# Optimization experiments

Measured on AMD Instinct MI355X. Metric: run time of the kernel, lower is better.

## Reference

```python
import math
import jax, jax.numpy as jnp
import numpy as np

D_MODEL = 2048
NUM_HEADS = 16

def setup_inputs() -> dict:
    key = jax.random.key(0)
    k1, k2, k3, k4, k5 = jax.random.split(key, 5)
    s = 1.0 / math.sqrt(D_MODEL)
    return {
        "in_features": jax.random.normal(k1, (2, 2048, D_MODEL), dtype=jnp.float32),
        "q_proj": jax.random.normal(k2, (D_MODEL, D_MODEL), dtype=jnp.float32) * s,
        "k_proj": jax.random.normal(k3, (D_MODEL, D_MODEL), dtype=jnp.float32) * s,
        "v_proj": jax.random.normal(k4, (D_MODEL, D_MODEL), dtype=jnp.float32) * s,
        "o_proj": jax.random.normal(k5, (D_MODEL, D_MODEL), dtype=jnp.float32) * s,
    }

def reference(in_features, q_proj, k_proj, v_proj, o_proj):
    B, S, D = in_features.shape
    H = NUM_HEADS
    d_k = D // H
    # x @ W.T, then split heads: [B, H, S, d_k]
    def proj(W):
        return (in_features @ W.T).reshape(B, S, H, d_k).transpose(0, 2, 1, 3)
    Q, K, V = proj(q_proj), proj(k_proj), proj(v_proj)
    scores = jnp.einsum("bhqd,bhkd->bhqk", Q, K) / math.sqrt(d_k)
    causal = jnp.triu(jnp.ones((S, S), dtype=bool), k=1)  # True above diagonal
    scores = jnp.where(causal, -jnp.inf, scores)
    attn = jax.nn.softmax(scores, axis=-1)
    out = jnp.einsum("bhqk,bhkd->bhqd", attn, V)
    out = out.transpose(0, 2, 1, 3).reshape(B, S, D)
    return out @ o_proj.T
```

## Files before the change

### kernel.cpp

```cpp
#include <hip/hip_runtime.h>
#include <math.h>
#include <stdint.h>

#define D_MODEL 2048
#define NHEAD   16
#define DK      128
#define SEQ     2048
#define BATCH   2
#define MROWS   (BATCH * SEQ)

typedef __bf16 bf16;
typedef __bf16 bf16x8 __attribute__((ext_vector_type(8)));
typedef __bf16 bf16x4 __attribute__((ext_vector_type(4)));
typedef float  f32x4  __attribute__((ext_vector_type(4)));

__device__ __forceinline__ bf16 f2bf(float f) {
    unsigned u = __builtin_bit_cast(unsigned, f);
    u += 0x7fffu + ((u >> 16) & 1u);
    unsigned short h = (unsigned short)(u >> 16);
    return __builtin_bit_cast(bf16, h);
}

#define GLDS16(gp, lp)                                                        \
    __builtin_amdgcn_global_load_lds(                                         \
        (__attribute__((address_space(1))) void*)(uintptr_t)(gp),             \
        (__attribute__((address_space(3))) void*)(lp), 16, 0, 0)

__global__ void cvt_f32_bf16(const float* __restrict__ src,
                             bf16* __restrict__ dst, int n4) {
    int i = blockIdx.x * blockDim.x + threadIdx.x;
    if (i < n4) {
        float4 v = ((const float4*)src)[i];
        bf16x4 o;
        o[0] = f2bf(v.x); o[1] = f2bf(v.y); o[2] = f2bf(v.z); o[3] = f2bf(v.w);
        *(bf16x4*)(dst + (size_t)i * 4) = o;
    }
}

template <int EPI>
__global__ __launch_bounds__(256)
void gemm_bt(const bf16* __restrict__ A, const bf16* __restrict__ B,
             void* __restrict__ Cv, int M, int N, int K) {
    __shared__ alignas(16) bf16 sA[128 * 32];
    __shared__ alignas(16) bf16 sB[128 * 32];

    const int tid  = threadIdx.x;
    const int lane = tid & 63;
    const int wid  = tid >> 6;
    const int wm   = wid >> 1, wn = wid & 1;
    const int brow = blockIdx.y * 128, bcol = blockIdx.x * 128;
    const int r16  = lane & 15, g = lane >> 4;

    f32x4 acc[4][4] = {};

    const int c0 = tid, c1 = 256 + tid;
    const int rowS0 = c0 >> 2, colS0 = (c0 & 3) * 8;
    const int rowS1 = c1 >> 2, colS1 = (c1 & 3) * 8;

    for (int kt = 0; kt < K; kt += 32) {
        GLDS16(A + (size_t)(brow + rowS0) * K + kt + colS0, &sA[c0 * 8]);
        GLDS16(A + (size_t)(brow + rowS1) * K + kt + colS1, &sA[c1 * 8]);
        GLDS16(B + (size_t)(bcol + rowS0) * K + kt + colS0, &sB[c0 * 8]);
        GLDS16(B + (size_t)(bcol + rowS1) * K + kt + colS1, &sB[c1 * 8]);
        __syncthreads();

        bf16x8 af[4], bfr[4];
#pragma unroll
        for (int m = 0; m < 4; ++m)
            af[m] = *(const bf16x8*)&sA[(wm * 64 + m * 16 + r16) * 32 + g * 8];
#pragma unroll
        for (int n = 0; n < 4; ++n)
            bfr[n] = *(const bf16x8*)&sB[(wn * 64 + n * 16 + r16) * 32 + g * 8];
#pragma unroll
        for (int m = 0; m < 4; ++m)
#pragma unroll
            for (int n = 0; n < 4; ++n)
                acc[m][n] = __builtin_amdgcn_mfma_f32_16x16x32_bf16(
                    af[m], bfr[n], acc[m][n], 0, 0, 0);
        __syncthreads();
    }

#pragma unroll
    for (int m = 0; m < 4; ++m) {
#pragma unroll
        for (int n = 0; n < 4; ++n) {
            const int col  = bcol + wn * 64 + n * 16 + r16;
            const int row0 = brow + wm * 64 + m * 16 + g * 4;
            if constexpr (EPI == 0) {
                bf16* C = (bf16*)Cv;
#pragma unroll
                for (int r = 0; r < 4; ++r)
                    C[(size_t)(row0 + r) * N + col] = f2bf(acc[m][n][r]);
            } else if constexpr (EPI == 1) {
                float* C = (float*)Cv;
#pragma unroll
                for (int r = 0; r < 4; ++r)
                    C[(size_t)(row0 + r) * N + col] = acc[m][n][r];
            } else {
                bf16* C = (bf16*)Cv;
                const int b = row0 >> 11, s = row0 & 2047;
                bf16x4 v;
#pragma unroll
                for (int r = 0; r < 4; ++r) v[r] = f2bf(acc[m][n][r]);
                *(bf16x4*)&C[(size_t)(b * 2048 + col) * 2048 + s] = v;
            }
        }
    }
}

__global__ __launch_bounds__(256)
void attn_fwd(const bf16* __restrict__ Q, const bf16* __restrict__ Kb,
              const bf16* __restrict__ Vt, bf16* __restrict__ AO) {
    __shared__ alignas(16) bf16 P_lds[4][32][40];

    const int tid  = threadIdx.x;
    const int lane = tid & 63;
    const int wid  = tid >> 6;
    const int r16  = lane & 15, g = lane >> 4;
    const int bh   = blockIdx.y;
    const int b    = bh >> 4;
    const int NT   = SEQ / 128;
    const int qt   = (blockIdx.y & 16) ? (NT - 1 - (int)blockIdx.x)
                                       : (int)blockIdx.x;
    const int qbase = qt * 128 + wid * 32;
    const size_t rowbase = (size_t)b * SEQ;
    const int hcol = (bh & 15) * DK;
    const float scale = 0.08838834764831845f;

    bf16x8 aq[2][4];
#pragma unroll
    for (int m = 0; m < 2; ++m) {
        const bf16* qp =
            Q + (rowbase + qbase + m * 16 + r16) * D_MODEL + hcol + g * 8;
#pragma unroll
        for (int c = 0; c < 4; ++c) aq[m][c] = *(const bf16x8*)(qp + c * 32);
    }

    f32x4 o[2][8] = {};
    float m_run[2][4], l_run[2][4];
#pragma unroll
    for (int m = 0; m < 2; ++m)
#pragma unroll
        for (int r = 0; r < 4; ++r) {
            m_run[m][r] = -INFINITY;
            l_run[m][r] = 0.f;
        }

    const int ntile = (qbase >> 5) + 1;
    for (int t = 0; t < ntile; ++t) {
        const int kv0 = t * 32;
        f32x4 s[2][2] = {};
#pragma unroll
        for (int n = 0; n < 2; ++n) {
            const bf16* kp =
                Kb + (rowbase + kv0 + n * 16 + r16) * D_MODEL + hcol + g * 8;
#pragma unroll
            for (int c = 0; c < 4; ++c) {
                bf16x8 bk = *(const bf16x8*)(kp + c * 32);
#pragma unroll
                for (int m = 0; m < 2; ++m)
                    s[m][n] = __builtin_amdgcn_mfma_f32_16x16x32_bf16(
                        aq[m][c], bk, s[m][n], 0, 0, 0);
            }
        }
#pragma unroll
        for (int m = 0; m < 2; ++m)
#pragma unroll
            for (int n = 0; n < 2; ++n)
#pragma unroll
                for (int r = 0; r < 4; ++r) s[m][n][r] *= scale;

        if (kv0 + 31 > qbase) {
#pragma unroll
            for (int m = 0; m < 2; ++m)
#pragma unroll
                for (int n = 0; n < 2; ++n)
#pragma unroll
                    for (int r = 0; r < 4; ++r) {
                        int kvg = kv0 + n * 16 + r16;
                        int qg  = qbase + m * 16 + g * 4 + r;
                        if (kvg > qg) s[m][n][r] = -INFINITY;
                    }
        }

        float tm[2][4];
#pragma unroll
        for (int m = 0; m < 2; ++m)
#pragma unroll
            for (int r = 0; r < 4; ++r) tm[m][r] = fmaxf(s[m][0][r], s[m][1][r]);
#pragma unroll
        for (int d = 1; d < 16; d <<= 1)
#pragma unroll
            for (int m = 0; m < 2; ++m)
#pragma unroll
                for (int r = 0; r < 4; ++r)
                    tm[m][r] = fmaxf(tm[m][r], __shfl_xor(tm[m][r], d));

        float alpha[2][4];
#pragma unroll
        for (int m = 0; m < 2; ++m)
#pragma unroll
            for (int r = 0; r < 4; ++r) {
                float nm    = fmaxf(m_run[m][r], tm[m][r]);
                alpha[m][r] = __expf(m_run[m][r] - nm);
                m_run[m][r] = nm;
            }
#pragma unroll
        for (int m = 0; m < 2; ++m)
#pragma unroll
            for (int n = 0; n < 2; ++n)
#pragma unroll
                for (int r = 0; r < 4; ++r)
                    s[m][n][r] = __expf(s[m][n][r] - m_run[m][r]);

        float rs[2][4];
#pragma unroll
        for (int m = 0; m < 2; ++m)
#pragma unroll
            for (int r = 0; r < 4; ++r) rs[m][r] = s[m][0][r] + s[m][1][r];
#pragma unroll
        for (int d = 1; d < 16; d <<= 1)
#pragma unroll
            for (int m = 0; m < 2; ++m)
#pragma unroll
                for (int r = 0; r < 4; ++r) rs[m][r] += __shfl_xor(rs[m][r], d);
#pragma unroll
        for (int m = 0; m < 2; ++m)
#pragma unroll
            for (int r = 0; r < 4; ++r)
                l_run[m][r] = l_run[m][r] * alpha[m][r] + rs[m][r];
#pragma unroll
        for (int m = 0; m < 2; ++m)
#pragma unroll
            for (int dt = 0; dt < 8; ++dt)
#pragma unroll
                for (int r = 0; r < 4; ++r) o[m][dt][r] *= alpha[m][r];

#pragma unroll
        for (int m = 0; m < 2; ++m)
#pragma unroll
            for (int n = 0; n < 2; ++n)
#pragma unroll
                for (int r = 0; r < 4; ++r)
                    P_lds[wid][m * 16 + g * 4 + r][n * 16 + r16] =
                        f2bf(s[m][n][r]);

        bf16x8 pa[2];
#pragma unroll
        for (int m = 0; m < 2; ++m)
            pa[m] = *(const bf16x8*)&P_lds[wid][m * 16 + r16][g * 8];

        const bf16* vp = Vt + ((size_t)bh * DK) * SEQ + kv0 + g * 8;
#pragma unroll
        for (int dt = 0; dt < 8; ++dt) {
            bf16x8 bv = *(const bf16x8*)(vp + (size_t)(dt * 16 + r16) * SEQ);
#pragma unroll
            for (int m = 0; m < 2; ++m)
                o[m][dt] = __builtin_amdgcn_mfma_f32_16x16x32_bf16(
                    pa[m], bv, o[m][dt], 0, 0, 0);
        }
    }

#pragma unroll
    for (int m = 0; m < 2; ++m) {
        float rl[4];
#pragma unroll
        for (int r = 0; r < 4; ++r) rl[r] = 1.f / l_run[m][r];
#pragma unroll
        for (int dt = 0; dt < 8; ++dt)
#pragma unroll
            for (int r = 0; r < 4; ++r) {
                float val = o[m][dt][r] * rl[r];
                AO[(rowbase + qbase + m * 16 + g * 4 + r) * D_MODEL + hcol +
                   dt * 16 + r16] = f2bf(val);
            }
    }
}

extern "C" void kernel_launch(void* const* d_in, const int* in_sizes, int n_in,
                              void* d_out, int out_size, void* d_ws,
                              size_t ws_size, hipStream_t stream) {
    const float* X  = (const float*)d_in[0];
    const float* Wq = (const float*)d_in[1];
    const float* Wk = (const float*)d_in[2];
    const float* Wv = (const float*)d_in[3];
    const float* Wo = (const float*)d_in[4];

    bf16* base = (bf16*)d_ws;
    const size_t NX = (size_t)MROWS * D_MODEL;
    const size_t NW = (size_t)D_MODEL * D_MODEL;
    bf16* Xb  = base;
    bf16* Qb  = Xb + NX;
    bf16* Kbf = Qb + NX;
    bf16* Vt  = Kbf + NX;
    bf16* AOb = Vt + NX;
    bf16* Wqb = AOb + NX;
    bf16* Wkb = Wqb + NW;
    bf16* Wvb = Wkb + NW;
    bf16* Wob = Wvb + NW;

    cvt_f32_bf16<<<(int)(NX / 4 / 256), 256, 0, stream>>>(X, Xb, (int)(NX / 4));
    cvt_f32_bf16<<<(int)(NW / 4 / 256), 256, 0, stream>>>(Wq, Wqb, (int)(NW / 4));
    cvt_f32_bf16<<<(int)(NW / 4 / 256), 256, 0, stream>>>(Wk, Wkb, (int)(NW / 4));
    cvt_f32_bf16<<<(int)(NW / 4 / 256), 256, 0, stream>>>(Wv, Wvb, (int)(NW / 4));
    cvt_f32_bf16<<<(int)(NW / 4 / 256), 256, 0, stream>>>(Wo, Wob, (int)(NW / 4));

    dim3 ggrid(D_MODEL / 128, MROWS / 128);
    gemm_bt<0><<<ggrid, 256, 0, stream>>>(Xb, Wqb, Qb, MROWS, D_MODEL, D_MODEL);
    gemm_bt<0><<<ggrid, 256, 0, stream>>>(Xb, Wkb, Kbf, MROWS, D_MODEL, D_MODEL);
    gemm_bt<2><<<ggrid, 256, 0, stream>>>(Xb, Wvb, Vt, MROWS, D_MODEL, D_MODEL);

    attn_fwd<<<dim3(SEQ / 128, BATCH * NHEAD), 256, 0, stream>>>(Qb, Kbf, Vt,
                                                                 AOb);

    gemm_bt<1><<<ggrid, 256, 0, stream>>>(AOb, Wob, d_out, MROWS, D_MODEL,
                                          D_MODEL);
}
```

Baseline: 547.4 us.

## Fuse QKV projections into one GEMM and stage K tiles in LDS for attention

Merges the three Q/K/V projection GEMMs into a single launch over a concatenated 6144-column weight, selecting the output path per block. The Q scale is folded into the Q epilogue so attention no longer multiplies scores. The attention kernel now processes 64-key tiles, double-buffers K into swizzled LDS with async global-to-LDS loads, and uses a finite large negative instead of -inf. This cuts launch count, improves K reuse across warps and widens the MFMA work per tile, at the cost of more LDS and registers per block. The fused GEMM indexes Wqb as one contiguous 6144x2048 weight, which holds only because Wq, Wk and Wv are laid out back to back in the buffer.

```diff
diff --git a/kernel.cpp b/kernel.cpp
--- a/kernel.cpp
+++ b/kernel.cpp
@@ -25,6 +25,8 @@
     __builtin_amdgcn_global_load_lds(                                         \
         (__attribute__((address_space(1))) void*)(uintptr_t)(gp),             \
         (__attribute__((address_space(3))) void*)(lp), 16, 0, 0)
+
+#define QSCALE 0.08838834764831845f
 
 __global__ void cvt_f32_bf16(const float* __restrict__ src,
                              bf16* __restrict__ dst, int n4) {
@@ -37,12 +39,13 @@
     }
 }
 
-template <int EPI>
 __global__ __launch_bounds__(256)
-void gemm_bt(const bf16* __restrict__ A, const bf16* __restrict__ B,
-             void* __restrict__ Cv, int M, int N, int K) {
+void gemm_qkv(const bf16* __restrict__ A, const bf16* __restrict__ B,
+              bf16* __restrict__ Qb, bf16* __restrict__ Kbf,
+              bf16* __restrict__ Vt) {
     __shared__ alignas(16) bf16 sA[128 * 32];
     __shared__ alignas(16) bf16 sB[128 * 32];
+    const int K = D_MODEL;
 
     const int tid  = threadIdx.x;
     const int lane = tid & 63;
@@ -80,38 +83,94 @@
         __syncthreads();
     }
 
+    const int which = bcol >> 11;
 #pragma unroll
     for (int m = 0; m < 4; ++m) {
 #pragma unroll
         for (int n = 0; n < 4; ++n) {
             const int col  = bcol + wn * 64 + n * 16 + r16;
             const int row0 = brow + wm * 64 + m * 16 + g * 4;
-            if constexpr (EPI == 0) {
-                bf16* C = (bf16*)Cv;
+            if (which == 0) {
 #pragma unroll
                 for (int r = 0; r < 4; ++r)
-                    C[(size_t)(row0 + r) * N + col] = f2bf(acc[m][n][r]);
-            } else if constexpr (EPI == 1) {
-                float* C = (float*)Cv;
+                    Qb[(size_t)(row0 + r) * D_MODEL + col] =
+                        f2bf(acc[m][n][r] * QSCALE);
+            } else if (which == 1) {
 #pragma unroll
                 for (int r = 0; r < 4; ++r)
-                    C[(size_t)(row0 + r) * N + col] = acc[m][n][r];
+                    Kbf[(size_t)(row0 + r) * D_MODEL + (col - 2048)] =
+                        f2bf(acc[m][n][r]);
             } else {
-                bf16* C = (bf16*)Cv;
                 const int b = row0 >> 11, s = row0 & 2047;
                 bf16x4 v;
 #pragma unroll
                 for (int r = 0; r < 4; ++r) v[r] = f2bf(acc[m][n][r]);
-                *(bf16x4*)&C[(size_t)(b * 2048 + col) * 2048 + s] = v;
+                *(bf16x4*)&Vt[(size_t)(b * 2048 + (col - 4096)) * 2048 + s] = v;
             }
         }
     }
 }
 
 __global__ __launch_bounds__(256)
+void gemm_o(const bf16* __restrict__ A, const bf16* __restrict__ B,
+            float* __restrict__ C) {
+    __shared__ alignas(16) bf16 sA[128 * 32];
+    __shared__ alignas(16) bf16 sB[128 * 32];
+    const int K = D_MODEL, N = D_MODEL;
+
+    const int tid  = threadIdx.x;
+    const int lane = tid & 63;
+    const int wid  = tid >> 6;
+    const int wm   = wid >> 1, wn = wid & 1;
+    const int brow = blockIdx.y * 128, bcol = blockIdx.x * 128;
+    const int r16  = lane & 15, g = lane >> 4;
+
+    f32x4 acc[4][4] = {};
+
+    const int c0 = tid, c1 = 256 + tid;
+    const int rowS0 = c0 >> 2, colS0 = (c0 & 3) * 8;
+    const int rowS1 = c1 >> 2, colS1 = (c1 & 3) * 8;
+
+    for (int kt = 0; kt < K; kt += 32) {
+        GLDS16(A + (size_t)(brow + rowS0) * K + kt + colS0, &sA[c0 * 8]);
+        GLDS16(A + (size_t)(brow + rowS1) * K + kt + colS1, &sA[c1 * 8]);
+        GLDS16(B + (size_t)(bcol + rowS0) * K + kt + colS0, &sB[c0 * 8]);
+        GLDS16(B + (size_t)(bcol + rowS1) * K + kt + colS1, &sB[c1 * 8]);
+        __syncthreads();
+
+        bf16x8 af[4], bfr[4];
+#pragma unroll
+        for (int m = 0; m < 4; ++m)
+            af[m] = *(const bf16x8*)&sA[(wm * 64 + m * 16 + r16) * 32 + g * 8];
+#pragma unroll
+        for (int n = 0; n < 4; ++n)
+            bfr[n] = *(const bf16x8*)&sB[(wn * 64 + n * 16 + r16) * 32 + g * 8];
+#pragma unroll
+        for (int m = 0; m < 4; ++m)
+#pragma unroll
+            for (int n = 0; n < 4; ++n)
+                acc[m][n] = __builtin_amdgcn_mfma_f32_16x16x32_bf16(
+                    af[m], bfr[n], acc[m][n], 0, 0, 0);
+        __syncthreads();
+    }
+
+#pragma unroll
+    for (int m = 0; m < 4; ++m)
+#pragma unroll
+        for (int n = 0; n < 4; ++n) {
+            const int col  = bcol + wn * 64 + n * 16 + r16;
+            const int row0 = brow + wm * 64 + m * 16 + g * 4;
+#pragma unroll
+            for (int r = 0; r < 4; ++r)
+                C[(size_t)(row0 + r) * N + col] = acc[m][n][r];
+        }
+}
+
+__global__ __launch_bounds__(256, 2)
 void attn_fwd(const bf16* __restrict__ Q, const bf16* __restrict__ Kb,
               const bf16* __restrict__ Vt, bf16* __restrict__ AO) {
-    __shared__ alignas(16) bf16 P_lds[4][32][40];
+    __shared__ alignas(16) bf16 sK[2][64 * 128];
+    __shared__ alignas(16) bf16 P_lds[4][32][72];
 
     const int tid  = threadIdx.x;
     const int lane = tid & 63;
@@ -119,13 +178,12 @@
     const int r16  = lane & 15, g = lane >> 4;
     const int bh   = blockIdx.y;
     const int b    = bh >> 4;
-    const int NT   = SEQ / 128;
-    const int qt   = (blockIdx.y & 16) ? (NT - 1 - (int)blockIdx.x)
+    const int qt   = (blockIdx.y & 16) ? (15 - (int)blockIdx.x)
                                        : (int)blockIdx.x;
     const int qbase = qt * 128 + wid * 32;
     const size_t rowbase = (size_t)b * SEQ;
     const int hcol = (bh & 15) * DK;
-    const float scale = 0.08838834764831845f;
+    const int nt   = 2 * qt + 2;
 
     bf16x8 aq[2][4];
 #pragma unroll
@@ -142,123 +200,159 @@
     for (int m = 0; m < 2; ++m)
 #pragma unroll
         for (int r = 0; r < 4; ++r) {
-            m_run[m][r] = -INFINITY;
+            m_run[m][r] = -3.0e38f;
             l_run[m][r] = 0.f;
         }
 
-    const int ntile = (qbase >> 5) + 1;
-    for (int t = 0; t < ntile; ++t) {
-        const int kv0 = t * 32;
-        f32x4 s[2][2] = {};
-#pragma unroll
-        for (int n = 0; n < 2; ++n) {
-            const bf16* kp =
-                Kb + (rowbase + kv0 + n * 16 + r16) * D_MODEL + hcol + g * 8;
+    auto stage = [&](int buf, int t) {
+        const int kv0 = t * 64;
+#pragma unroll
+        for (int j = 0; j < 4; ++j) {
+            const int ldsOff = wid * 1024 + j * 4096 + lane * 16;
+            const int row    = ldsOff >> 8;
+            const int colB   = (lane & 15) * 16;
+            const int scolB  = colB ^ ((row & 7) << 4);
+            const bf16* gp =
+                Kb + (rowbase + kv0 + row) * D_MODEL + hcol + (scolB >> 1);
+            GLDS16(gp, (bf16*)sK[buf] + (ldsOff >> 1));
+        }
+    };
+
+    int cur = 0;
+    stage(0, 0);
+    __syncthreads();
+
+    for (int t = 0; t < nt; ++t) {
+        if (t + 1 < nt) stage(cur ^ 1, t + 1);
+        const int kv0 = t * 64;
+
+        if (kv0 <= qbase + 31) {
+            f32x4 s[2][4] = {};
 #pragma unroll
             for (int c = 0; c < 4; ++c) {
-                bf16x8 bk = *(const bf16x8*)(kp + c * 32);
+                bf16x8 kf[4];
+#pragma unroll
+                for (int n = 0; n < 4; ++n) {
+                    const int row  = n * 16 + r16;
+                    const int colB = (c * 64 + g * 16) ^ ((row & 7) << 4);
+                    kf[n] = *(const bf16x8*)&sK[cur][row * 128 + (colB >> 1)];
+                }
+#pragma unroll
+                for (int n = 0; n < 4; ++n)
+#pragma unroll
+                    for (int m = 0; m < 2; ++m)
+                        s[m][n] = __builtin_amdgcn_mfma_f32_16x16x32_bf16(
+                            aq[m][c], kf[n], s[m][n], 0, 0, 0);
+            }
+
+            if (kv0 + 63 > qbase) {
 #pragma unroll
                 for (int m = 0; m < 2; ++m)
-                    s[m][n] = __builtin_amdgcn_mfma_f32_16x16x32_bf16(
-                        aq[m][c], bk, s[m][n], 0, 0, 0);
+#pragma unroll
+                    for (int n = 0; n < 4; ++n)
+#pragma unroll
+                        for (int r = 0; r < 4; ++r) {
+                            int kvg = kv0 + n * 16 + r16;
+                            int qg  = qbase + m * 16 + g * 4 + r;
+                            if (kvg > qg) s[m][n][r] = -3.0e38f;
+                        }
+            }
+
+            float tm[2][4];
+#pragma unroll
+            for (int m = 0; m < 2; ++m)
+#pragma unroll
+                for (int r = 0; r < 4; ++r)
+                    tm[m][r] = fmaxf(fmaxf(s[m][0][r], s[m][1][r]),
+                                     fmaxf(s[m][2][r], s[m][3][r]));
+#pragma unroll
+            for (int d = 1; d < 16; d <<= 1)
+#pragma unroll
+                for (int m = 0; m < 2; ++m)
+#pragma unroll
+                    for (int r = 0; r < 4; ++r)
+                        tm[m][r] = fmaxf(tm[m][r], __shfl_xor(tm[m][r], d));
+
+            float alpha[2][4];
+#pragma unroll
+            for (int m = 0; m < 2; ++m)
+#pragma unroll
+                for (int r = 0; r < 4; ++r) {
+                    float nm    = fmaxf(m_run[m][r], tm[m][r]);
+                    alpha[m][r] = __expf(m_run[m][r] - nm);
+                    m_run[m][r] = nm;
+                }
+#pragma unroll
+            for (int m = 0; m < 2; ++m)
+#pragma unroll
+                for (int n = 0; n < 4; ++n)
+#pragma unroll
+                    for (int r = 0; r < 4; ++r)
+                        s[m][n][r] = __expf(s[m][n][r] - m_run[m][r]);
+
+            float rs[2][4];
+#pragma unroll
+            for (int m = 0; m < 2; ++m)
+#pragma unroll
+                for (int r = 0; r < 4; ++r)
+                    rs[m][r] = (s[m][0][r] + s[m][1][r]) +
+                               (s[m][2][r] + s[m][3][r]);
+#pragma unroll
+            for (int d = 1; d < 16; d <<= 1)
+#pragma unroll
+                for (int m = 0; m < 2; ++m)
+#pragma unroll
+                    for (int r = 0; r < 4; ++r)
+                        rs[m][r] += __shfl_xor(rs[m][r], d);
+#pragma unroll
+            for (int m = 0; m < 2; ++m)
+#pragma unroll
+                for (int r = 0; r < 4; ++r)
+                    l_run[m][r] = l_run[m][r] * alpha[m][r] + rs[m][r];
+#pragma unroll
+            for (int m = 0; m < 2; ++m)
+#pragma unroll
+                for (int dt = 0; dt < 8; ++dt)
+#pragma unroll
+                    for (int r = 0; r < 4; ++r) o[m][dt][r] *= alpha[m][r];
+
+#pragma unroll
+            for (int m = 0; m < 2; ++m)
+#pragma unroll
+                for (int n = 0; n < 4; ++n)
+#pragma unroll
+                    for (int r = 0; r < 4; ++r)
+                        P_lds[wid][m * 16 + g * 4 + r][n * 16 + r16] =
+                            f2bf(s[m][n][r]);
+
+            bf16x8 pa[2][2];
+#pragma unroll
+            for (int m = 0; m < 2; ++m)
+#pragma unroll
+                for (int c = 0; c < 2; ++c)
+                    pa[m][c] = *(const bf16x8*)&P_lds[wid][m * 16 + r16]
+                                                    [c * 32 + g * 8];
+
+            const bf16* vp = Vt + ((size_t)bh * DK) * SEQ + kv0 + g * 8;
+#pragma unroll
+            for (int dt = 0; dt < 8; ++dt) {
+                bf16x8 bv[2];
+#pragma unroll
+                for (int c = 0; c < 2; ++c)
+                    bv[c] = *(const bf16x8*)(vp +
+                                             (size_t)(dt * 16 + r16) * SEQ +
+                                             c * 32);
+#pragma unroll
+                for (int m = 0; m < 2; ++m)
+#pragma unroll
+                    for (int c = 0; c < 2; ++c)
+                        o[m][dt] = __builtin_amdgcn_mfma_f32_16x16x32_bf16(
+                            pa[m][c], bv[c], o[m][dt], 0, 0, 0);
             }
         }
-#pragma unroll
-        for (int m = 0; m < 2; ++m)
-#pragma unroll
-            for (int n = 0; n < 2; ++n)
-#pragma unroll
-                for (int r = 0; r < 4; ++r) s[m][n][r] *= scale;
-
-        if (kv0 + 31 > qbase) {
-#pragma unroll
-            for (int m = 0; m < 2; ++m)
-#pragma unroll
-                for (int n = 0; n < 2; ++n)
-#pragma unroll
-                    for (int r = 0; r < 4; ++r) {
-                        int kvg = kv0 + n * 16 + r16;
-                        int qg  = qbase + m * 16 + g * 4 + r;
-                        if (kvg > qg) s[m][n][r] = -INFINITY;
-                    }
-        }
-
-        float tm[2][4];
-#pragma unroll
-        for (int m = 0; m < 2; ++m)
-#pragma unroll
-            for (int r = 0; r < 4; ++r) tm[m][r] = fmaxf(s[m][0][r], s[m][1][r]);
-#pragma unroll
-        for (int d = 1; d < 16; d <<= 1)
-#pragma unroll
-            for (int m = 0; m < 2; ++m)
-#pragma unroll
-                for (int r = 0; r < 4; ++r)
-                    tm[m][r] = fmaxf(tm[m][r], __shfl_xor(tm[m][r], d));
-
-        float alpha[2][4];
-#pragma unroll
-        for (int m = 0; m < 2; ++m)
-#pragma unroll
-            for (int r = 0; r < 4; ++r) {
-                float nm    = fmaxf(m_run[m][r], tm[m][r]);
-                alpha[m][r] = __expf(m_run[m][r] - nm);
-                m_run[m][r] = nm;
-            }
-#pragma unroll
-        for (int m = 0; m < 2; ++m)
-#pragma unroll
-            for (int n = 0; n < 2; ++n)
-#pragma unroll
-                for (int r = 0; r < 4; ++r)
-                    s[m][n][r] = __expf(s[m][n][r] - m_run[m][r]);
-
-        float rs[2][4];
-#pragma unroll
-        for (int m = 0; m < 2; ++m)
-#pragma unroll
-            for (int r = 0; r < 4; ++r) rs[m][r] = s[m][0][r] + s[m][1][r];
-#pragma unroll
-        for (int d = 1; d < 16; d <<= 1)
-#pragma unroll
-            for (int m = 0; m < 2; ++m)
-#pragma unroll
-                for (int r = 0; r < 4; ++r) rs[m][r] += __shfl_xor(rs[m][r], d);
-#pragma unroll
-        for (int m = 0; m < 2; ++m)
-#pragma unroll
-            for (int r = 0; r < 4; ++r)
-                l_run[m][r] = l_run[m][r] * alpha[m][r] + rs[m][r];
-#pragma unroll
-        for (int m = 0; m < 2; ++m)
-#pragma unroll
-            for (int dt = 0; dt < 8; ++dt)
-#pragma unroll
-                for (int r = 0; r < 4; ++r) o[m][dt][r] *= alpha[m][r];
-
-#pragma unroll
-        for (int m = 0; m < 2; ++m)
-#pragma unroll
-            for (int n = 0; n < 2; ++n)
-#pragma unroll
-                for (int r = 0; r < 4; ++r)
-                    P_lds[wid][m * 16 + g * 4 + r][n * 16 + r16] =
-                        f2bf(s[m][n][r]);
-
-        bf16x8 pa[2];
-#pragma unroll
-        for (int m = 0; m < 2; ++m)
-            pa[m] = *(const bf16x8*)&P_lds[wid][m * 16 + r16][g * 8];
-
-        const bf16* vp = Vt + ((size_t)bh * DK) * SEQ + kv0 + g * 8;
-#pragma unroll
-        for (int dt = 0; dt < 8; ++dt) {
-            bf16x8 bv = *(const bf16x8*)(vp + (size_t)(dt * 16 + r16) * SEQ);
-#pragma unroll
-            for (int m = 0; m < 2; ++m)
-                o[m][dt] = __builtin_amdgcn_mfma_f32_16x16x32_bf16(
-                    pa[m], bv, o[m][dt], 0, 0, 0);
-        }
+
+        __syncthreads();
+        cur ^= 1;
     }
 
 #pragma unroll
@@ -305,14 +399,10 @@
     cvt_f32_bf16<<<(int)(NW / 4 / 256), 256, 0, stream>>>(Wv, Wvb, (int)(NW / 4));
     cvt_f32_bf16<<<(int)(NW / 4 / 256), 256, 0, stream>>>(Wo, Wob, (int)(NW / 4));
 
-    dim3 ggrid(D_MODEL / 128, MROWS / 128);
-    gemm_bt<0><<<ggrid, 256, 0, stream>>>(Xb, Wqb, Qb, MROWS, D_MODEL, D_MODEL);
-    gemm_bt<0><<<ggrid, 256, 0, stream>>>(Xb, Wkb, Kbf, MROWS, D_MODEL, D_MODEL);
-    gemm_bt<2><<<ggrid, 256, 0, stream>>>(Xb, Wvb, Vt, MROWS, D_MODEL, D_MODEL);
+    gemm_qkv<<<dim3(48, 32), 256, 0, stream>>>(Xb, Wqb, Qb, Kbf, Vt);
 
     attn_fwd<<<dim3(SEQ / 128, BATCH * NHEAD), 256, 0, stream>>>(Qb, Kbf, Vt,
                                                                  AOb);
 
-    gemm_bt<1><<<ggrid, 256, 0, stream>>>(AOb, Wob, d_out, MROWS, D_MODEL,
-                                          D_MODEL);
-}
+    gemm_o<<<dim3(16, 32), 256, 0, stream>>>(AOb, Wob, (float*)d_out);
+}
```

Result: faster. 531.9 us (-2.8%).
